# Kernel optimization log

Measured on AMD Instinct MI355X. Metric: run time of the kernel, lower is better.

## Reference

```python
import jax, jax.numpy as jnp
import numpy as np

B, T, V, D = 64, 2048, 32000, 256  # batch, seq_len, vocab, emb_dim == hidden_size
H = D
NUM_CLASSES = 27
N_NODES = 128


def setup_inputs() -> dict:
    key = jax.random.key(0)
    ks = jax.random.split(key, 8)
    s = 1.0 / np.sqrt(D)
    return {
        "tokens": jax.random.randint(ks[0], (B, T), 0, V),
        "node_token_span_starts": jax.random.randint(ks[1], (B, N_NODES), 0, T),
        "node_token_span_ends": jax.random.randint(ks[2], (B, N_NODES), 0, T),
        "embed": jax.random.normal(ks[3], (V, D), dtype=jnp.float32),
        "Wi": jax.random.normal(ks[4], (D, 4 * H), dtype=jnp.float32) * s,
        "Wh": jax.random.normal(ks[5], (H, 4 * H), dtype=jnp.float32) * s,
        "bh": jnp.zeros((4 * H,), dtype=jnp.float32),
        "Wo": jax.random.normal(ks[6], (H, NUM_CLASSES), dtype=jnp.float32) * s,
        "bo": jnp.zeros((NUM_CLASSES,), dtype=jnp.float32),
    }


def reference(tokens, node_token_span_starts, node_token_span_ends,
              embed, Wi, Wh, bh, Wo, bo):
    # node_token_span_* are unused by the original forward (dead code).
    x = embed[tokens.astype(jnp.int32)]            # [B, T, D]
    # Precompute input projections for all timesteps in one big GEMM.
    zx = jnp.einsum('btd,df->btf', x, Wi) + bh     # [B, T, 4H]
    batch = tokens.shape[0]
    c0 = jnp.zeros((batch, H), dtype=x.dtype)
    h0 = jnp.zeros((batch, H), dtype=x.dtype)

    def step(carry, zxt):
        c, h = carry
        z = zxt + h @ Wh                           # [B, 4H]
        i, f, g, o = jnp.split(z, 4, axis=-1)
        c = jax.nn.sigmoid(f) * c + jax.nn.sigmoid(i) * jnp.tanh(g)
        h = jax.nn.sigmoid(o) * jnp.tanh(c)
        return (c, h), h

    (c, h), _ = jax.lax.scan(step, (c0, h0), jnp.swapaxes(zx, 0, 1))
    # forward_outputs[:, -1, :] == final hidden state h
    return h @ Wo + bo                             # [B, NUM_CLASSES]
```

## Files before the change

kernel.cpp:

```cpp
#include <hip/hip_runtime.h>
#include <hip/hip_bf16.h>
#include <stdint.h>

typedef __hip_bfloat16 bf16;
typedef __attribute__((ext_vector_type(8))) short short8;
typedef __attribute__((ext_vector_type(4))) float f32x4;
typedef __attribute__((ext_vector_type(4))) int i32x4;
typedef __attribute__((ext_vector_type(2))) int i32x2;
typedef __attribute__((ext_vector_type(4))) unsigned int u32x4;

#define NB   64
#define NT   2048
#define NV   32000
#define ND   256
#define NH4  1024
#define NCLS 27


__global__ __launch_bounds__(256) void k_cvt_embed(const float* __restrict__ e,
                                                   bf16* __restrict__ o) {
  int i = blockIdx.x * blockDim.x + threadIdx.x;
  float4 v = reinterpret_cast<const float4*>(e)[i];
  union { bf16 h[4]; uint2 u; } pk;
  pk.h[0] = __float2bfloat16(v.x);
  pk.h[1] = __float2bfloat16(v.y);
  pk.h[2] = __float2bfloat16(v.z);
  pk.h[3] = __float2bfloat16(v.w);
  reinterpret_cast<uint2*>(o)[i] = pk.u;
}

__global__ __launch_bounds__(256) void k_cvt_wi(const float* __restrict__ wi,
                                                bf16* __restrict__ wit) {
  int i = blockIdx.x * blockDim.x + threadIdx.x;
  int col = i >> 8;
  int k   = i & 255;
  wit[i] = __float2bfloat16(wi[k * NH4 + col]);
}

__global__ __launch_bounds__(256) void k_scale(const float* __restrict__ wh,
                                               float* __restrict__ dq,
                                               float* __restrict__ rdq,
                                               float* __restrict__ rw) {
  int col = blockIdx.x * 256 + threadIdx.x;
  float m = 0.f;
  for (int k = 0; k < ND; ++k) m = fmaxf(m, fabsf(wh[k * NH4 + col]));
  dq[col]  = m * (1.f / 16129.f);
  rdq[col] = 16129.f / m;
  rw[col]  = 127.f / m;
}

__global__ __launch_bounds__(256) void k_cvt_whq(const float* __restrict__ wh,
                                                 const float* __restrict__ rw,
                                                 signed char* __restrict__ whq) {
  int idx  = blockIdx.x * 256 + threadIdx.x;
  int ii   = idx & 15;
  int lane = (idx >> 4) & 63;
  int kq   = (idx >> 10) & 3;
  int nt   = idx >> 12;
  int k   = kq * 64 + (lane >> 4) * 16 + ii;
  int col = nt * 16 + (lane & 15);
  whq[idx] = (signed char)(int)rintf(wh[k * NH4 + col] * rw[col]);
}

__global__ __launch_bounds__(256) void k_gemm_zx(const int*  __restrict__ tokens,
                                                 const bf16* __restrict__ eb,
                                                 const bf16* __restrict__ wit,
                                                 const float* __restrict__ rdq,
                                                 int* __restrict__ zxq,
                                                 int t0, int lgch) {
  __shared__ bf16 As[4 * 64 * 8];
  __shared__ bf16 Bs[4 * 64 * 8];
  int bid  = blockIdx.x;
  int nb   = bid & 15;
  int mb   = bid >> 4;
  int n0   = nb * 64;
  int tid  = threadIdx.x, lane = tid & 63, wave = tid >> 6;
  int wm   = wave >> 1, wn = wave & 1;
  int srow = tid >> 2;
  int skg  = tid & 3;

  long trow = (long)tokens[srow * NT + t0 + mb] * ND;
  const bf16* ap = eb  + trow + skg * 8;
  const bf16* bp = wit + (long)(n0 + srow) * ND + skg * 8;
  bf16* as_dst = &As[(skg * 64 + srow) * 8];
  bf16* bs_dst = &Bs[(skg * 64 + srow) * 8];

  f32x4 acc[2][2] = {};
  for (int k0 = 0; k0 < ND; k0 += 32) {
    __syncthreads();
    *(u32x4*)as_dst = *(const u32x4*)(ap + k0);
    *(u32x4*)bs_dst = *(const u32x4*)(bp + k0);
    __syncthreads();
    short8 a0 = *(const short8*)&As[((lane >> 4) * 64 + wm * 32 +  0 + (lane & 15)) * 8];
    short8 a1 = *(const short8*)&As[((lane >> 4) * 64 + wm * 32 + 16 + (lane & 15)) * 8];
    short8 b0 = *(const short8*)&Bs[((lane >> 4) * 64 + wn * 32 +  0 + (lane & 15)) * 8];
    short8 b1 = *(const short8*)&Bs[((lane >> 4) * 64 + wn * 32 + 16 + (lane & 15)) * 8];
    acc[0][0] = __builtin_amdgcn_mfma_f32_16x16x32_bf16(a0, b0, acc[0][0], 0, 0, 0);
    acc[0][1] = __builtin_amdgcn_mfma_f32_16x16x32_bf16(a0, b1, acc[0][1], 0, 0, 0);
    acc[1][0] = __builtin_amdgcn_mfma_f32_16x16x32_bf16(a1, b0, acc[1][0], 0, 0, 0);
    acc[1][1] = __builtin_amdgcn_mfma_f32_16x16x32_bf16(a1, b1, acc[1][1], 0, 0, 0);
  }

  int cb  = n0 + wn * 32 + (lane & 15);
  float rq0 = rdq[cb], rq1 = rdq[cb + 16];
  int bb = wm * 32 + (lane >> 4) * 4;
#pragma unroll
  for (int fm = 0; fm < 2; ++fm) {
    int b0r = bb + fm * 16;
    int p0  = b0r >> 1;
#pragma unroll
    for (int fn = 0; fn < 2; ++fn) {
      int col = cb + fn * 16;
      int nt  = col >> 4;
      float rq = fn ? rq1 : rq0;
      int v0 = (int)rintf(acc[fm][fn][0] * rq);
      int v1 = (int)rintf(acc[fm][fn][1] * rq);
      int v2 = (int)rintf(acc[fm][fn][2] * rq);
      int v3 = (int)rintf(acc[fm][fn][3] * rq);
      size_t base = ((size_t)(p0 << lgch) + mb) * 2048 + nt * 32 + (col & 15) * 2;
      i32x2 w01; w01[0] = v0; w01[1] = v1;
      i32x2 w23; w23[0] = v2; w23[1] = v3;
      *(i32x2*)(zxq + base) = w01;
      *(i32x2*)(zxq + base + ((size_t)1 << lgch) * 2048) = w23;
    }
  }
}

__device__ __forceinline__ float sigf(float x) {
  return __builtin_amdgcn_rcpf(1.f + __expf(-x));
}
__device__ __forceinline__ float tanh_fast(float x) {
  return 1.f - 2.f * __builtin_amdgcn_rcpf(1.f + __expf(2.f * x));
}

#define LSTM_STEP(Z, ST)                                                        \
  {                                                                             \
    i32x4 a0 = *(const i32x4*)&aF[0 * 1024 + l * 16];                           \
    i32x4 a1 = *(const i32x4*)&aF[1 * 1024 + l * 16];                           \
    i32x4 a2 = *(const i32x4*)&aF[2 * 1024 + l * 16];                           \
    i32x4 a3 = *(const i32x4*)&aF[3 * 1024 + l * 16];                           \
    i32x4 acc[8];                                                               \
    _Pragma("unroll")                                                           \
    for (int j = 0; j < 8; ++j) {                                               \
      i32x4 zc; zc[0] = Z[j][0]; zc[1] = Z[j][1]; zc[2] = 0; zc[3] = 0;         \
      i32x4 t;                                                                  \
      t = __builtin_amdgcn_mfma_i32_16x16x64_i8(a0, w[j][0], zc, 0, 0, 0);      \
      t = __builtin_amdgcn_mfma_i32_16x16x64_i8(a1, w[j][1], t, 0, 0, 0);       \
      t = __builtin_amdgcn_mfma_i32_16x16x64_i8(a2, w[j][2], t, 0, 0, 0);       \
      acc[j] = __builtin_amdgcn_mfma_i32_16x16x64_i8(a3, w[j][3], t, 0, 0, 0);  \
    }                                                                           \
    if ((ST) + 2 < tn) {                                                        \
      const int* zn = zb + (size_t)((ST) + 2) * 2048;                           \
      _Pragma("unroll")                                                         \
      for (int j = 0; j < 8; ++j)                                               \
        Z[j] = *(const i32x2*)(zn + (wv * 8 + j) * 32);                         \
    }                                                                           \
    if (l4 == 0) {                                                              \
      _Pragma("unroll")                                                         \
      for (int j = 0; j < 8; ++j) {                                             \
        int col = (wv * 8 + j) * 16 + l15;                                      \
        int tt  = ((col & 255) << 2) | (col >> 8);                              \
        zl[tt]        = acc[j][0];                                              \
        zl[1024 + tt] = acc[j][1];                                              \
      }                                                                         \
    }                                                                           \
    __syncthreads();                                                            \
    {                                                                           \
      i32x4 zr = *(const i32x4*)&zl[b * 1024 + u * 4];                          \
      float zi = (float)zr[0] * dqv[0] + bhv[0];                                \
      float zf = (float)zr[1] * dqv[1] + bhv[1];                                \
      float zg = (float)zr[2] * dqv[2] + bhv[2];                                \
      float zo = (float)zr[3] * dqv[3] + bhv[3];                                \
      c = sigf(zf) * c + sigf(zi) * tanh_fast(zg);                              \
      float h = sigf(zo) * tanh_fast(c);                                        \
      aF[kqu * 1024 + (b | (lgu << 4)) * 16 + iiu] =                            \
          (signed char)(int)rintf(h * 127.f);                                   \
      if ((ST) == tn - 1) hst[(p * 2 + b) * 256 + u] = h;                       \
    }                                                                           \
    __syncthreads();                                                            \
  }

__global__ __launch_bounds__(512, 1) void k_lstm(const int* __restrict__ zxq,
                                                 const signed char* __restrict__ whq,
                                                 const float* __restrict__ dq,
                                                 const float* __restrict__ bh,
                                                 float* __restrict__ cst,
                                                 float* __restrict__ hst,
                                                 int t0, int tn, int lgch) {
  __shared__ int  zl[2 * 1024];
  __shared__ signed char aF[4 * 64 * 16];

  int p   = blockIdx.x;
  int tid = threadIdx.x;
  int l   = tid & 63;
  int wv  = tid >> 6;
  int l15 = l & 15, l4 = l >> 4;
  int u   = tid & 255;
  int b   = tid >> 8;

  i32x4 w[8][4];
#pragma unroll
  for (int j = 0; j < 8; ++j) {
    int nt = wv * 8 + j;
#pragma unroll
    for (int kq = 0; kq < 4; ++kq)
      w[j][kq] = *(const i32x4*)&whq[((nt * 4 + kq) * 64 + l) * 16];
  }
#pragma unroll
  for (int j = 0; j < 8; ++j)
#pragma unroll
    for (int kq = 0; kq < 4; ++kq)
      asm volatile("" : "+v"(w[j][kq]));

  float dqv[4], bhv[4];
#pragma unroll
  for (int q = 0; q < 4; ++q) { dqv[q] = dq[q * 256 + u]; bhv[q] = bh[q * 256 + u]; }
  float c = (t0 == 0) ? 0.f : cst[(p * 2 + b) * 256 + u];

  int kqu = u >> 6, lgu = (u >> 4) & 3, iiu = u & 15;

  if (tid < 256) ((i32x4*)aF)[tid] = (i32x4)0;
  __syncthreads();
  if (t0 != 0) {
    int hq = (int)rintf(hst[(p * 2 + b) * 256 + u] * 127.f);
    aF[kqu * 1024 + (b | (lgu << 4)) * 16 + iiu] = (signed char)hq;
  }
  __syncthreads();

  const int* zb = zxq + ((size_t)(p << lgch)) * 2048 + l15 * 2;
  i32x2 zA[8], zB[8];
#pragma unroll
  for (int j = 0; j < 8; ++j) {
    zA[j] = *(const i32x2*)(zb + (wv * 8 + j) * 32);
    zB[j] = *(const i32x2*)(zb + 2048 + (wv * 8 + j) * 32);
  }

  for (int lt = 0; lt < tn; lt += 2) {
    LSTM_STEP(zA, lt)
    LSTM_STEP(zB, lt + 1)
  }

  cst[(p * 2 + b) * 256 + u] = c;
}

__global__ __launch_bounds__(64) void k_out(const float* __restrict__ hfin,
                                            const float* __restrict__ wo,
                                            const float* __restrict__ bo,
                                            float* __restrict__ y) {
  __shared__ float hsm[256];
  int b = blockIdx.x, tid = threadIdx.x;
  for (int i = tid; i < 256; i += 64) hsm[i] = hfin[b * 256 + i];
  __syncthreads();
  if (tid < NCLS) {
    float s = bo[tid];
    for (int k = 0; k < 256; ++k) s += hsm[k] * wo[k * NCLS + tid];
    y[b * NCLS + tid] = s;
  }
}

extern "C" void kernel_launch(void* const* d_in, const int* in_sizes, int n_in,
                              void* d_out, int out_size, void* d_ws, size_t ws_size,
                              hipStream_t stream) {
  const int*   tokens = (const int*)d_in[0];
  const float* embed  = (const float*)d_in[3];
  const float* wi     = (const float*)d_in[4];
  const float* wh     = (const float*)d_in[5];
  const float* bh     = (const float*)d_in[6];
  const float* wo     = (const float*)d_in[7];
  const float* bo     = (const float*)d_in[8];
  float* y = (float*)d_out;

  char* ws = (char*)d_ws;
  bf16* eb        = (bf16*)ws;        ws += (size_t)NV * ND * 2;
  bf16* wit       = (bf16*)ws;        ws += (size_t)NH4 * ND * 2;
  signed char* whq = (signed char*)ws; ws += (size_t)ND * NH4;
  float* dqv      = (float*)ws;       ws += (size_t)NH4 * 4;
  float* rdq      = (float*)ws;       ws += (size_t)NH4 * 4;
  float* rw       = (float*)ws;       ws += (size_t)NH4 * 4;
  float* cst      = (float*)ws;       ws += (size_t)NB * ND * 4;
  float* hst      = (float*)ws;       ws += (size_t)NB * ND * 4;
  size_t fixed = (size_t)(ws - (char*)d_ws);

  int CHUNK = 32, lgch = 5;
  static const int cand[]  = {512, 256, 128, 64, 32};
  static const int candl[] = {9, 8, 7, 6, 5};
  for (int ci = 0; ci < 5; ++ci) {
    size_t need = fixed + (size_t)cand[ci] * 262144;
    if (need <= ws_size) { CHUNK = cand[ci]; lgch = candl[ci]; break; }
  }
  int* zxq = (int*)ws;

  hipLaunchKernelGGL(k_cvt_embed, dim3(NV * ND / 4 / 256), dim3(256), 0, stream, embed, eb);
  hipLaunchKernelGGL(k_cvt_wi,    dim3(NH4 * ND / 256), dim3(256), 0, stream, wi, wit);
  hipLaunchKernelGGL(k_scale,     dim3(4), dim3(256), 0, stream, wh, dqv, rdq, rw);
  hipLaunchKernelGGL(k_cvt_whq,   dim3(1024), dim3(256), 0, stream, wh, rw, whq);

  for (int t0 = 0; t0 < NT; t0 += CHUNK) {
    hipLaunchKernelGGL(k_gemm_zx, dim3(CHUNK * 16), dim3(256), 0, stream,
                       tokens, eb, wit, rdq, zxq, t0, lgch);
    hipLaunchKernelGGL(k_lstm, dim3(32), dim3(512), 0, stream,
                       zxq, whq, dqv, bh, cst, hst, t0, CHUNK, lgch);
  }
  hipLaunchKernelGGL(k_out, dim3(NB), dim3(64), 0, stream, hst, wo, bo, y);
}
```

Baseline: 2.281 ms.

## Add input projection in elementwise phase instead of MFMA accumulator seed

The precomputed input projection zx is now stored in a per-(batch,unit) gate-interleaved layout. Each thread loads one i32x4 per step and adds it to the recurrent MFMA result after the LDS exchange, instead of seeding the MFMA accumulators with per-fragment values. This shrinks the per-thread register footprint from 16 i32x2 prefetch registers to two i32x4 and simplifies the MFMA chain to start from a zero accumulator. The cost is scattered scalar stores in the GEMM epilogue, which may slow the projection kernel.

```diff
diff --git a/kernel.cpp b/kernel.cpp
--- a/kernel.cpp
+++ b/kernel.cpp
@@ -6,7 +6,6 @@
 typedef __attribute__((ext_vector_type(8))) short short8;
 typedef __attribute__((ext_vector_type(4))) float f32x4;
 typedef __attribute__((ext_vector_type(4))) int i32x4;
-typedef __attribute__((ext_vector_type(2))) int i32x2;
 typedef __attribute__((ext_vector_type(4))) unsigned int u32x4;
 
 #define NB   64
@@ -106,22 +105,18 @@
   int bb = wm * 32 + (lane >> 4) * 4;
 #pragma unroll
   for (int fm = 0; fm < 2; ++fm) {
-    int b0r = bb + fm * 16;
-    int p0  = b0r >> 1;
 #pragma unroll
     for (int fn = 0; fn < 2; ++fn) {
       int col = cb + fn * 16;
-      int nt  = col >> 4;
+      int uu  = col & 255, q = col >> 8;
       float rq = fn ? rq1 : rq0;
-      int v0 = (int)rintf(acc[fm][fn][0] * rq);
-      int v1 = (int)rintf(acc[fm][fn][1] * rq);
-      int v2 = (int)rintf(acc[fm][fn][2] * rq);
-      int v3 = (int)rintf(acc[fm][fn][3] * rq);
-      size_t base = ((size_t)(p0 << lgch) + mb) * 2048 + nt * 32 + (col & 15) * 2;
-      i32x2 w01; w01[0] = v0; w01[1] = v1;
-      i32x2 w23; w23[0] = v2; w23[1] = v3;
-      *(i32x2*)(zxq + base) = w01;
-      *(i32x2*)(zxq + base + ((size_t)1 << lgch) * 2048) = w23;
+#pragma unroll
+      for (int i2 = 0; i2 < 4; ++i2) {
+        int rr = bb + fm * 16 + i2;
+        int p0 = rr >> 1;
+        size_t idx = (((size_t)(p0 << lgch) + mb) * 2 + (rr & 1)) * 1024 + uu * 4 + q;
+        zxq[idx] = (int)rintf(acc[fm][fn][i2] * rq);
+      }
     }
   }
 }
@@ -133,7 +128,7 @@
   return 1.f - 2.f * __builtin_amdgcn_rcpf(1.f + __expf(2.f * x));
 }
 
-#define LSTM_STEP(Z, ST)                                                        \
+#define LSTM_STEP(ZX, ST)                                                       \
   {                                                                             \
     i32x4 a0 = *(const i32x4*)&aF[0 * 1024 + l * 16];                           \
     i32x4 a1 = *(const i32x4*)&aF[1 * 1024 + l * 16];                           \
@@ -142,18 +137,11 @@
     i32x4 acc[8];                                                               \
     _Pragma("unroll")                                                           \
     for (int j = 0; j < 8; ++j) {                                               \
-      i32x4 zc; zc[0] = Z[j][0]; zc[1] = Z[j][1]; zc[2] = 0; zc[3] = 0;         \
       i32x4 t;                                                                  \
-      t = __builtin_amdgcn_mfma_i32_16x16x64_i8(a0, w[j][0], zc, 0, 0, 0);      \
+      t = __builtin_amdgcn_mfma_i32_16x16x64_i8(a0, w[j][0], czero, 0, 0, 0);   \
       t = __builtin_amdgcn_mfma_i32_16x16x64_i8(a1, w[j][1], t, 0, 0, 0);       \
       t = __builtin_amdgcn_mfma_i32_16x16x64_i8(a2, w[j][2], t, 0, 0, 0);       \
       acc[j] = __builtin_amdgcn_mfma_i32_16x16x64_i8(a3, w[j][3], t, 0, 0, 0);  \
-    }                                                                           \
-    if ((ST) + 2 < tn) {                                                        \
-      const int* zn = zb + (size_t)((ST) + 2) * 2048;                           \
-      _Pragma("unroll")                                                         \
-      for (int j = 0; j < 8; ++j)                                               \
-        Z[j] = *(const i32x2*)(zn + (wv * 8 + j) * 32);                         \
     }                                                                           \
     if (l4 == 0) {                                                              \
       _Pragma("unroll")                                                         \
@@ -167,11 +155,17 @@
     __syncthreads();                                                            \
     {                                                                           \
       i32x4 zr = *(const i32x4*)&zl[b * 1024 + u * 4];                          \
-      float zi = (float)zr[0] * dqv[0] + bhv[0];                                \
-      float zf = (float)zr[1] * dqv[1] + bhv[1];                                \
-      float zg = (float)zr[2] * dqv[2] + bhv[2];                                \
-      float zo = (float)zr[3] * dqv[3] + bhv[3];                                \
-      c = sigf(zf) * c + sigf(zi) * tanh_fast(zg);                              \
+      int s0 = zr[0] + ZX[0];                                                   \
+      int s1 = zr[1] + ZX[1];                                                   \
+      int s2 = zr[2] + ZX[2];                                                   \
+      int s3 = zr[3] + ZX[3];                                                   \
+      if ((ST) + 2 < tn)                                                        \
+        ZX = *(const i32x4*)(zg + (size_t)((ST) + 2) * 2048);                   \
+      float zi = (float)s0 * dqv[0] + bhv[0];                                   \
+      float zf = (float)s1 * dqv[1] + bhv[1];                                   \
+      float zg_ = (float)s2 * dqv[2] + bhv[2];                                  \
+      float zo = (float)s3 * dqv[3] + bhv[3];                                   \
+      c = sigf(zf) * c + sigf(zi) * tanh_fast(zg_);                             \
       float h = sigf(zo) * tanh_fast(c);                                        \
       aF[kqu * 1024 + (b | (lgu << 4)) * 16 + iiu] =                            \
           (signed char)(int)rintf(h * 127.f);                                   \
@@ -212,6 +206,9 @@
     for (int kq = 0; kq < 4; ++kq)
       asm volatile("" : "+v"(w[j][kq]));
 
+  i32x4 czero = (i32x4)0;
+  asm volatile("" : "+v"(czero));
+
   float dqv[4], bhv[4];
 #pragma unroll
   for (int q = 0; q < 4; ++q) { dqv[q] = dq[q * 256 + u]; bhv[q] = bh[q * 256 + u]; }
@@ -227,17 +224,13 @@
   }
   __syncthreads();
 
-  const int* zb = zxq + ((size_t)(p << lgch)) * 2048 + l15 * 2;
-  i32x2 zA[8], zB[8];
-#pragma unroll
-  for (int j = 0; j < 8; ++j) {
-    zA[j] = *(const i32x2*)(zb + (wv * 8 + j) * 32);
-    zB[j] = *(const i32x2*)(zb + 2048 + (wv * 8 + j) * 32);
-  }
+  const int* zg = zxq + ((size_t)(p << lgch) * 2 + b) * 1024 + u * 4;
+  i32x4 zxA = *(const i32x4*)zg;
+  i32x4 zxB = *(const i32x4*)(zg + 2048);
 
   for (int lt = 0; lt < tn; lt += 2) {
-    LSTM_STEP(zA, lt)
-    LSTM_STEP(zB, lt + 1)
+    LSTM_STEP(zxA, lt)
+    LSTM_STEP(zxB, lt + 1)
   }
 
   cst[(p * 2 + b) * 256 + u] = c;
```

Result: faster. 2.229 ms (-2.3%).
